# Optimization experiments

Hardware: AMD Instinct MI355X
Metric: run time of the kernel (lower is better)

## Reference

```python
import jax, jax.numpy as jnp
import numpy as np

B, S, H = 1, 2048, 4096
NH, DN, DR, DV = 32, 128, 64, 128   # heads, nope dim, rope dim, v dim
QK = DN + DR                         # 192
RQ, RKV = 1536, 512
EPS = 1e-6
NEG = jnp.float32(-1e9)


def rmsnorm(x, w, eps=EPS):
    x32 = x.astype(jnp.float32)
    var = jnp.mean(x32 * x32, axis=-1, keepdims=True)
    return (x32 * jax.lax.rsqrt(var + eps)).astype(x.dtype) * w


def rope_complex(x, cos, sin):
    # x: [..., S, D]; interpret adjacent pairs as complex, multiply by e^{i*theta}
    xr, xi = x[..., 0::2], x[..., 1::2]
    or_ = xr * cos - xi * sin
    oi_ = xr * sin + xi * cos
    return jnp.stack([or_, oi_], axis=-1).reshape(x.shape)


def setup_inputs() -> dict:
    key = jax.random.key(0)
    ks = jax.random.split(key, 8)
    std = 0.02
    # RoPE angles: theta_j = pos * base^{-2j/DR}, shape [B, S, DR/2]
    inv_freq = 1.0 / (10000.0 ** (np.arange(0, DR, 2, dtype=np.float32) / DR))
    pos = np.arange(S, dtype=np.float32)
    freqs = jnp.asarray(np.broadcast_to(pos[:, None] * inv_freq[None, :], (B, S, DR // 2)))
    return {
        "hidden_states": jax.random.normal(ks[0], (B, S, H), jnp.float32),
        "freqs": freqs,
        "q_a_w": jax.random.normal(ks[1], (RQ, H), jnp.float32) * std,
        "q_a_ln_w": jnp.ones((RQ,), jnp.float32),
        "q_b_w": jax.random.normal(ks[2], (NH * QK, RQ), jnp.float32) * std,
        "kv_a_w": jax.random.normal(ks[3], (RKV + DR, H), jnp.float32) * std,
        "kv_a_ln_w": jnp.ones((RKV,), jnp.float32),
        "kv_b_w": jax.random.normal(ks[4], (NH * (DN + DV), RKV), jnp.float32) * std,
        "o_w": jax.random.normal(ks[5], (H, NH * DV), jnp.float32) * std,
    }


def reference(hidden_states, freqs, q_a_w, q_a_ln_w, q_b_w, kv_a_w, kv_a_ln_w, kv_b_w, o_w):
    b, s, _ = hidden_states.shape
    # --- low-rank Q: hidden -> q_lora_rank -> heads*(nope+rope) ---
    q = rmsnorm(hidden_states @ q_a_w.T, q_a_ln_w) @ q_b_w.T          # [B,S,NH*QK]
    q = q.reshape(b, s, NH, QK).transpose(0, 2, 1, 3)                  # [B,NH,S,QK]
    q_pass, q_rot = q[..., :DN], q[..., DN:]                           # [B,NH,S,DN],[B,NH,S,DR]
    # --- compressed KV + shared rope key ---
    ckv = hidden_states @ kv_a_w.T                                     # [B,S,RKV+DR]
    k_pass_c, k_rot = ckv[..., :RKV], ckv[..., RKV:]
    kv = rmsnorm(k_pass_c, kv_a_ln_w) @ kv_b_w.T                       # [B,S,NH*(DN+DV)]
    kv = kv.reshape(b, s, NH, DN + DV).transpose(0, 2, 1, 3)           # [B,NH,S,DN+DV]
    k_pass, v = kv[..., :DN], kv[..., DN:]
    k_rot = k_rot.reshape(b, 1, s, DR)                                 # [B,1,S,DR]
    # --- decoupled RoPE (complex form) ---
    cos = jnp.cos(freqs)[:, None]                                      # [B,1,S,DR/2]
    sin = jnp.sin(freqs)[:, None]
    q_rot = rope_complex(q_rot, cos, sin)
    k_rot = rope_complex(k_rot, cos, sin)
    k_rot = jnp.broadcast_to(k_rot, (b, NH, s, DR))
    query = jnp.concatenate([q_pass, q_rot], axis=-1)                  # [B,NH,S,QK]
    key = jnp.concatenate([k_pass, k_rot], axis=-1)
    # --- causal attention ---
    scaling = QK ** -0.5
    scores = jnp.einsum("bhqd,bhkd->bhqk", query, key) * scaling
    causal = jnp.tril(jnp.ones((s, s), bool))
    scores = jnp.where(causal, scores, NEG)
    probs = jax.nn.softmax(scores.astype(jnp.float32), axis=-1).astype(query.dtype)
    out = jnp.einsum("bhqk,bhkd->bhqd", probs, v)                      # [B,NH,S,DV]
    out = out.transpose(0, 2, 1, 3).reshape(b, s, NH * DV)
    return out @ o_w.T                                                 # [B,S,H]
```

## Files before the change

### kernel.cpp

```cpp
#include <hip/hip_runtime.h>
#define S_LEN 2048
#define HDIM 4096
#define NHEAD 32
#define QKD 192
#define RQ_ 1536
#define CKV_W 576
#define KVW 8192
#define QFW 6144
#define SC2F 0.1041216313667742f

typedef float f32x4 __attribute__((ext_vector_type(4)));
typedef __bf16 bf16x8 __attribute__((ext_vector_type(8)));

__device__ __forceinline__ unsigned short f2bf(float f) {
  unsigned int u = __float_as_uint(f);
  u += 0x7fffu + ((u >> 16) & 1u);
  return (unsigned short)(u >> 16);
}
__device__ __forceinline__ float b2f(unsigned short u) {
  return __uint_as_float((unsigned int)u << 16);
}
__device__ __forceinline__ float ex2(float x) { return exp2f(x); }

__device__ __forceinline__ void stage16(const void* g, void* lds_base, int lane) {
  __builtin_amdgcn_global_load_lds(
      (const __attribute__((address_space(1))) unsigned int*)g,
      (__attribute__((address_space(3))) unsigned int*)lds_base, 16, 0, 0);
}

__global__ __launch_bounds__(256) void cvt_kernel(
    const float* __restrict__ in, unsigned short* __restrict__ out, int n8) {
  int i = blockIdx.x * 256 + threadIdx.x;
  if (i >= n8) return;
  const float4* p = reinterpret_cast<const float4*>(in) + (size_t)i * 2;
  float4 a = p[0], b = p[1];
  unsigned long long lo = (unsigned long long)f2bf(a.x) | ((unsigned long long)f2bf(a.y) << 16)
      | ((unsigned long long)f2bf(a.z) << 32) | ((unsigned long long)f2bf(a.w) << 48);
  unsigned long long hi = (unsigned long long)f2bf(b.x) | ((unsigned long long)f2bf(b.y) << 16)
      | ((unsigned long long)f2bf(b.z) << 32) | ((unsigned long long)f2bf(b.w) << 48);
  unsigned long long* q = reinterpret_cast<unsigned long long*>(out) + (size_t)i * 2;
  q[0] = lo; q[1] = hi;
}

template<bool BF16OUT, bool SPLITK, bool VSCAT>
__global__ __launch_bounds__(256) void gemm_bf(
    const unsigned short* __restrict__ A, int lda,
    const unsigned short* __restrict__ B, int ldb,
    void* __restrict__ Cv, int ldc, int N, int K,
    unsigned short* __restrict__ VtOut) {
  __shared__ unsigned short As[2][4][128][8];
  __shared__ unsigned short Bs[2][4][128][8];
  const int tid = threadIdx.x, lane = tid & 63, w = tid >> 6;
  const int gx = (int)gridDim.x, gy = (int)gridDim.y;
  const int nwg = gx * gy;
  int lin = (int)blockIdx.y * gx + (int)blockIdx.x;
  if ((nwg & 7) == 0) lin = (lin & 7) * (nwg >> 3) + (lin >> 3);
  const int bm = (lin % gy) * 128, bn = (lin / gy) * 128;
  const int koff = SPLITK ? (int)blockIdx.z * K : 0;
  const int wr = (w >> 1) * 64, wc = (w & 1) * 64;
  const int lg = lane >> 4, lm = lane & 15;
  f32x4 acc[4][4] = {};
  const int arow = bm + lane;
  int brow = bn + lane; if (brow >= N) brow = N - 1;

  auto STAGE = [&](int buf, int k0) {
#pragma unroll
    for (int i = 0; i < 2; ++i) {
      stage16(A + (size_t)(arow + i * 64) * lda + koff + k0 + w * 8, &As[buf][w][i * 64][0], lane);
      int br2 = brow + i * 64; if (br2 >= N) br2 = N - 1;
      stage16(B + (size_t)br2 * ldb + koff + k0 + w * 8, &Bs[buf][w][i * 64][0], lane);
    }
  };
  STAGE(0, 0);
  __syncthreads();
  int cur = 0;
  for (int k0 = 0; k0 < K; k0 += 32) {
    if (k0 + 32 < K) STAGE(cur ^ 1, k0 + 32);
    bf16x8 af[4], bf[4];
#pragma unroll
    for (int i = 0; i < 4; ++i)
      af[i] = *reinterpret_cast<const bf16x8*>(&As[cur][lg][wr + i * 16 + lm][0]);
#pragma unroll
    for (int j = 0; j < 4; ++j)
      bf[j] = *reinterpret_cast<const bf16x8*>(&Bs[cur][lg][wc + j * 16 + lm][0]);
    __builtin_amdgcn_s_setprio(1);
#pragma unroll
    for (int i = 0; i < 4; ++i)
#pragma unroll
      for (int j = 0; j < 4; ++j)
        acc[i][j] = __builtin_amdgcn_mfma_f32_16x16x32_bf16(af[i], bf[j], acc[i][j], 0, 0, 0);
    __builtin_amdgcn_s_setprio(0);
    __syncthreads();
    cur ^= 1;
  }

  if constexpr (VSCAT) {
    if (bn & 128) {
      const int h2 = bn >> 8;
#pragma unroll
      for (int i = 0; i < 4; ++i)
#pragma unroll
        for (int j = 0; j < 4; ++j) {
          int d = wc + j * 16 + lm;
          unsigned long long pk =
                (unsigned long long)f2bf(acc[i][j][0])
              | ((unsigned long long)f2bf(acc[i][j][1]) << 16)
              | ((unsigned long long)f2bf(acc[i][j][2]) << 32)
              | ((unsigned long long)f2bf(acc[i][j][3]) << 48);
          *reinterpret_cast<unsigned long long*>(
              VtOut + (size_t)(h2 * 128 + d) * S_LEN + bm + wr + i * 16 + lg * 4) = pk;
        }
      return;
    }
  }

  size_t zoff = SPLITK ? (size_t)blockIdx.z * S_LEN * N : 0;
#pragma unroll
  for (int i = 0; i < 4; ++i)
#pragma unroll
    for (int j = 0; j < 4; ++j)
#pragma unroll
      for (int r = 0; r < 4; ++r) {
        int row = bm + wr + i * 16 + lg * 4 + r;
        int col = bn + wc + j * 16 + lm;
        if (col < N) {
          if constexpr (BF16OUT)
            ((unsigned short*)Cv)[(size_t)row * ldc + col] = f2bf(acc[i][j][r]);
          else
            ((float*)Cv)[zoff + (size_t)row * ldc + col] = acc[i][j][r];
        }
      }
}

__global__ __launch_bounds__(256) void rms_sum_q(
    const float* __restrict__ P, const float* __restrict__ w,
    unsigned short* __restrict__ y) {
  __shared__ float red[4];
  const int row = blockIdx.x, tid = threadIdx.x;
  const float* base = P + (size_t)row * RQ_;
  float x[6]; float ss = 0.f;
#pragma unroll
  for (int ii = 0; ii < 6; ++ii) {
    int j = tid + ii * 256;
    float v = 0.f;
#pragma unroll
    for (int z = 0; z < 4; ++z) v += base[(size_t)z * S_LEN * RQ_ + j];
    x[ii] = v; ss += v * v;
  }
#pragma unroll
  for (int off = 1; off < 64; off <<= 1) ss += __shfl_xor(ss, off, 64);
  if ((tid & 63) == 0) red[tid >> 6] = ss;
  __syncthreads();
  float scale = rsqrtf((red[0] + red[1] + red[2] + red[3]) / (float)RQ_ + 1e-6f);
  unsigned short* q = y + (size_t)row * RQ_;
#pragma unroll
  for (int ii = 0; ii < 6; ++ii) {
    int j = tid + ii * 256;
    q[j] = f2bf(x[ii] * scale * w[j]);
  }
}

__global__ __launch_bounds__(256) void rms_sum_kv(
    const float* __restrict__ P, const float* __restrict__ w,
    unsigned short* __restrict__ y, float* __restrict__ rotf) {
  __shared__ float red[4];
  const int row = blockIdx.x, tid = threadIdx.x;
  const float* base = P + (size_t)row * CKV_W;
  float x0 = 0.f, x1 = 0.f, x2 = 0.f;
#pragma unroll
  for (int z = 0; z < 8; ++z) {
    const float* b = base + (size_t)z * S_LEN * CKV_W;
    x0 += b[tid]; x1 += b[tid + 256];
    if (tid < 64) x2 += b[tid + 512];
  }
  float ss = x0 * x0 + x1 * x1;
#pragma unroll
  for (int off = 1; off < 64; off <<= 1) ss += __shfl_xor(ss, off, 64);
  if ((tid & 63) == 0) red[tid >> 6] = ss;
  __syncthreads();
  float scale = rsqrtf((red[0] + red[1] + red[2] + red[3]) / 512.0f + 1e-6f);
  unsigned short* q = y + (size_t)row * 512;
  q[tid] = f2bf(x0 * scale * w[tid]);
  q[tid + 256] = f2bf(x1 * scale * w[tid + 256]);
  if (tid < 64) rotf[(size_t)row * 64 + tid] = x2;
}

__global__ __launch_bounds__(256) void rope_q_kernel(
    unsigned short* __restrict__ qf, const float* __restrict__ freqs) {
  int idx = blockIdx.x * 256 + threadIdx.x;
  if (idx >= NHEAD * S_LEN * 32) return;
  int r = idx & 31, s = (idx >> 5) & (S_LEN - 1), h = idx >> 16;
  unsigned short* p = qf + (size_t)s * QFW + h * QKD + 128 + 2 * r;
  float xr = b2f(p[0]), xi = b2f(p[1]);
  float f = freqs[(size_t)s * 32 + r];
  float c = cosf(f), sn = sinf(f);
  *reinterpret_cast<unsigned int*>(p) =
      (unsigned int)f2bf(xr * c - xi * sn) | ((unsigned int)f2bf(xr * sn + xi * c) << 16);
}

__global__ __launch_bounds__(256) void rope_k_kernel(
    const float* __restrict__ rotf, const float* __restrict__ freqs,
    unsigned short* __restrict__ Kr) {
  int idx = blockIdx.x * 256 + threadIdx.x;
  if (idx >= S_LEN * 32) return;
  int r = idx & 31, s = idx >> 5;
  float xr = rotf[(size_t)s * 64 + 2 * r];
  float xi = rotf[(size_t)s * 64 + 2 * r + 1];
  float f = freqs[(size_t)s * 32 + r];
  float c = cosf(f), sn = sinf(f);
  *reinterpret_cast<unsigned int*>(Kr + (size_t)s * 64 + 2 * r) =
      (unsigned int)f2bf(xr * c - xi * sn) | ((unsigned int)f2bf(xr * sn + xi * c) << 16);
}

__global__ __launch_bounds__(256, 3) void attn_kernel(
    const unsigned short* __restrict__ Qf,
    const unsigned short* __restrict__ KV,
    const unsigned short* __restrict__ Kr,
    const unsigned short* __restrict__ Vt,
    unsigned short* __restrict__ O) {
  __shared__ unsigned short Ks[2][32 * 192];
  __shared__ unsigned short Vs[2][128 * 32];
  __shared__ unsigned short Ps[4][16 * 32];
  const int tid = threadIdx.x, lane = tid & 63, w = tid >> 6;
  const int wg = (int)blockIdx.x;
  const int lin = (wg & 7) * 128 + (wg >> 3);
  const int h = lin >> 5;
  const int qt = 31 - (lin & 31);
  const int qr0 = qt * 64 + w * 16;
  const int lg = lane >> 4, lm = lane & 15, lm7 = lane & 7;
  const unsigned short* Qh = Qf + h * QKD;
  const int hoff = h * 256;
  const unsigned short* Vh = Vt + (size_t)h * 128 * S_LEN;

  bf16x8 qf[6];
#pragma unroll
  for (int f = 0; f < 6; ++f)
    qf[f] = *reinterpret_cast<const bf16x8*>(
        Qh + (size_t)(qr0 + lm) * QFW + f * 32 + lg * 8);

  f32x4 o[8] = {};
  float l[4] = {};

  auto STAGE = [&](int b, int kp) {
#pragma unroll
    for (int i = 0; i < 3; ++i) {
      int fb = (w * 3 + i) * 64 + lane;
      int row = fb / 24;
      int blk = fb - row * 24;
      int gb = (blk & ~7) | ((blk ^ row) & 7);
      const unsigned short* src = (blk < 16)
          ? KV + (size_t)(kp + row) * KVW + hoff + gb * 8
          : Kr + (size_t)(kp + row) * 64 + (gb - 16) * 8;
      stage16(src, &Ks[b][(w * 3 + i) * 512], lane);
    }
#pragma unroll
    for (int i = 0; i < 2; ++i) {
      int fb = (w * 2 + i) * 64 + lane;
      int row = fb >> 2;
      int blk = fb & 3;
      stage16(Vh + (size_t)row * S_LEN + kp + blk * 8, &Vs[b][(w * 2 + i) * 512], lane);
    }
  };

  const int ntiles = (qt + 1) * 2;
  STAGE(0, 0);
  __syncthreads();
  int buf = 0;
  for (int ti = 0; ti < ntiles; ++ti) {
    const int kp = ti * 32;
    if (ti + 1 < ntiles) STAGE(buf ^ 1, kp + 32);
    if (kp <= qr0 + 15) {
      f32x4 sc[2] = {};
      __builtin_amdgcn_s_setprio(1);
#pragma unroll
      for (int f = 0; f < 6; ++f)
#pragma unroll
        for (int c = 0; c < 2; ++c) {
          int blk = f * 4 + lg;
          int sb = (blk & ~7) | ((blk ^ lm7) & 7);
          bf16x8 kf = *reinterpret_cast<const bf16x8*>(&Ks[buf][(c * 16 + lm) * 192 + sb * 8]);
          sc[c] = __builtin_amdgcn_mfma_f32_16x16x32_bf16(qf[f], kf, sc[c], 0, 0, 0);
        }
      __builtin_amdgcn_s_setprio(0);
      const int rb = qr0 + lg * 4;
#pragma unroll
      for (int r = 0; r < 4; ++r) {
        const int row = rb + r;
        float v0 = fmaf(sc[0][r], SC2F, -32.f); if (kp + lm > row) v0 = -1e9f;
        float v1 = fmaf(sc[1][r], SC2F, -32.f); if (kp + 16 + lm > row) v1 = -1e9f;
        float p0 = ex2(v0), p1 = ex2(v1);
        l[r] += p0 + p1;
        int pr = lg * 4 + r;
        int s3 = pr & 3;
        int b0 = lm >> 3;
        unsigned short* pp = &Ps[w][pr * 32];
        pp[((b0 ^ s3) << 3) + lm7] = f2bf(p0);
        pp[(((2 + b0) ^ s3) << 3) + lm7] = f2bf(p1);
      }
      bf16x8 pa = *reinterpret_cast<const bf16x8*>(
          &Ps[w][lm * 32 + ((lg ^ (lm & 3)) << 3)]);
      __builtin_amdgcn_s_setprio(1);
#pragma unroll
      for (int d = 0; d < 8; ++d) {
        bf16x8 vf = *reinterpret_cast<const bf16x8*>(&Vs[buf][(d * 16 + lm) * 32 + lg * 8]);
        o[d] = __builtin_amdgcn_mfma_f32_16x16x32_bf16(pa, vf, o[d], 0, 0, 0);
      }
      __builtin_amdgcn_s_setprio(0);
    }
    __syncthreads();
    buf ^= 1;
  }
#pragma unroll
  for (int r = 0; r < 4; ++r) {
    float t = l[r];
#pragma unroll
    for (int off = 1; off < 16; off <<= 1) t += __shfl_xor(t, off, 16);
    float inv = 1.0f / t;
    int row = qr0 + lg * 4 + r;
#pragma unroll
    for (int d = 0; d < 8; ++d)
      O[(size_t)row * 4096 + h * 128 + d * 16 + lm] = f2bf(o[d][r] * inv);
  }
}

extern "C" void kernel_launch(void* const* d_in, const int* in_sizes, int n_in,
                              void* d_out, int out_size, void* d_ws, size_t ws_size,
                              hipStream_t stream) {
  const float* hs = (const float*)d_in[0];
  const float* freqs = (const float*)d_in[1];
  const float* q_a_w = (const float*)d_in[2];
  const float* q_a_ln = (const float*)d_in[3];
  const float* q_b_w = (const float*)d_in[4];
  const float* kv_a_w = (const float*)d_in[5];
  const float* kv_a_ln = (const float*)d_in[6];
  const float* kv_b_w = (const float*)d_in[7];
  const float* o_w = (const float*)d_in[8];
  float* out = (float*)d_out;

  char* ws = (char*)d_ws;
  unsigned short* wslot = (unsigned short*)(ws + 0);
  unsigned short* hs_bf = (unsigned short*)(ws + 33554432);
  unsigned short* attnb = (unsigned short*)(ws + 33554432);
  float* qa_part = (float*)(ws + 50331648);
  unsigned short* kv_bf = (unsigned short*)(ws + 50331648);
  float* ckv_part = (float*)(ws + 100663296);
  unsigned short* qa_bf = (unsigned short*)(ws + 138412032);
  unsigned short* ckv_bf = (unsigned short*)(ws + 144703488);
  float* rotf = (float*)(ws + 146800640);
  unsigned short* qfullb = (unsigned short*)(ws + 147324928);
  unsigned short* Vt = (unsigned short*)(ws + 172490752);
  unsigned short* Kr = (unsigned short*)(ws + 189267968);

  dim3 blk(256);
  auto cvt = [&](const float* src, unsigned short* dst, size_t n) {
    int n8 = (int)(n / 8);
    cvt_kernel<<<(n8 + 255) / 256, blk, 0, stream>>>(src, dst, n8);
  };

  cvt(hs, hs_bf, (size_t)S_LEN * HDIM);
  cvt(q_a_w, wslot, (size_t)RQ_ * HDIM);
  gemm_bf<false, true, false><<<dim3(RQ_ / 128, S_LEN / 128, 4), blk, 0, stream>>>(
      hs_bf, HDIM, wslot, HDIM, qa_part, RQ_, RQ_, HDIM / 4, nullptr);
  cvt(kv_a_w, wslot, (size_t)CKV_W * HDIM);
  gemm_bf<false, true, false><<<dim3((CKV_W + 127) / 128, S_LEN / 128, 8), blk, 0, stream>>>(
      hs_bf, HDIM, wslot, HDIM, ckv_part, CKV_W, CKV_W, HDIM / 8, nullptr);
  rms_sum_q<<<S_LEN, blk, 0, stream>>>(qa_part, q_a_ln, qa_bf);
  rms_sum_kv<<<S_LEN, blk, 0, stream>>>(ckv_part, kv_a_ln, ckv_bf, rotf);
  cvt(q_b_w, wslot, (size_t)QFW * RQ_);
  gemm_bf<true, false, false><<<dim3(QFW / 128, S_LEN / 128), blk, 0, stream>>>(
      qa_bf, RQ_, wslot, RQ_, qfullb, QFW, QFW, RQ_, nullptr);
  cvt(kv_b_w, wslot, (size_t)KVW * 512);
  gemm_bf<true, false, true><<<dim3(KVW / 128, S_LEN / 128), blk, 0, stream>>>(
      ckv_bf, 512, wslot, 512, kv_bf, KVW, KVW, 512, Vt);
  rope_q_kernel<<<(NHEAD * S_LEN * 32 + 255) / 256, blk, 0, stream>>>(qfullb, freqs);
  rope_k_kernel<<<(S_LEN * 32 + 255) / 256, blk, 0, stream>>>(rotf, freqs, Kr);
  attn_kernel<<<dim3(1024), blk, 0, stream>>>(qfullb, kv_bf, Kr, Vt, attnb);
  cvt(o_w, wslot, (size_t)HDIM * HDIM);
  gemm_bf<false, false, false><<<dim3(HDIM / 128, S_LEN / 128), blk, 0, stream>>>(
      attnb, HDIM, wslot, HDIM, out, HDIM, HDIM, HDIM, nullptr);
}
```

Measured before the change: 523.7 us.

## Merge q_a and kv_a projections into one split-K GEMM and fuse k-rope into rmsnorm

Concatenates the q_a and kv_a weights in the workspace so a single split-K GEMM (17 column tiles, 4 K-splits) computes both low-rank projections into one partial buffer. The KV normalisation kernel now applies RoPE to the shared rope key directly using a lane shuffle, which removes the separate rope_k kernel and its fp32 intermediate. This cuts kernel launches and fills the GPU better than two small GEMMs. In exchange, the kv part now uses 4 K-splits instead of 8, and the last column tile is partially masked.

```diff
diff --git a/kernel.cpp b/kernel.cpp
--- a/kernel.cpp
+++ b/kernel.cpp
@@ -5,6 +5,7 @@
 #define QKD 192
 #define RQ_ 1536
 #define CKV_W 576
+#define NQKV 2112
 #define KVW 8192
 #define QFW 6144
 #define SC2F 0.1041216313667742f
@@ -137,14 +138,14 @@
     unsigned short* __restrict__ y) {
   __shared__ float red[4];
   const int row = blockIdx.x, tid = threadIdx.x;
-  const float* base = P + (size_t)row * RQ_;
+  const float* base = P + (size_t)row * NQKV;
   float x[6]; float ss = 0.f;
 #pragma unroll
   for (int ii = 0; ii < 6; ++ii) {
     int j = tid + ii * 256;
     float v = 0.f;
 #pragma unroll
-    for (int z = 0; z < 4; ++z) v += base[(size_t)z * S_LEN * RQ_ + j];
+    for (int z = 0; z < 4; ++z) v += base[(size_t)z * S_LEN * NQKV + j];
     x[ii] = v; ss += v * v;
   }
 #pragma unroll
@@ -162,14 +163,15 @@
 
 __global__ __launch_bounds__(256) void rms_sum_kv(
     const float* __restrict__ P, const float* __restrict__ w,
-    unsigned short* __restrict__ y, float* __restrict__ rotf) {
+    const float* __restrict__ freqs,
+    unsigned short* __restrict__ y, unsigned short* __restrict__ Kr) {
   __shared__ float red[4];
   const int row = blockIdx.x, tid = threadIdx.x;
-  const float* base = P + (size_t)row * CKV_W;
+  const float* base = P + (size_t)row * NQKV + RQ_;
   float x0 = 0.f, x1 = 0.f, x2 = 0.f;
 #pragma unroll
-  for (int z = 0; z < 8; ++z) {
-    const float* b = base + (size_t)z * S_LEN * CKV_W;
+  for (int z = 0; z < 4; ++z) {
+    const float* b = base + (size_t)z * S_LEN * NQKV;
     x0 += b[tid]; x1 += b[tid + 256];
     if (tid < 64) x2 += b[tid + 512];
   }
@@ -182,7 +184,15 @@
   unsigned short* q = y + (size_t)row * 512;
   q[tid] = f2bf(x0 * scale * w[tid]);
   q[tid + 256] = f2bf(x1 * scale * w[tid + 256]);
-  if (tid < 64) rotf[(size_t)row * 64 + tid] = x2;
+  if (tid < 64) {
+    float part = __shfl_xor(x2, 1, 64);
+    int r = tid >> 1;
+    float f = freqs[(size_t)row * 32 + r];
+    float c = cosf(f), sn = sinf(f);
+    float out = (tid & 1) ? (part * sn + x2 * c)
+                          : (x2 * c - part * sn);
+    Kr[(size_t)row * 64 + tid] = f2bf(out);
+  }
 }
 
 __global__ __launch_bounds__(256) void rope_q_kernel(
@@ -195,20 +205,6 @@
   float f = freqs[(size_t)s * 32 + r];
   float c = cosf(f), sn = sinf(f);
   *reinterpret_cast<unsigned int*>(p) =
-      (unsigned int)f2bf(xr * c - xi * sn) | ((unsigned int)f2bf(xr * sn + xi * c) << 16);
-}
-
-__global__ __launch_bounds__(256) void rope_k_kernel(
-    const float* __restrict__ rotf, const float* __restrict__ freqs,
-    unsigned short* __restrict__ Kr) {
-  int idx = blockIdx.x * 256 + threadIdx.x;
-  if (idx >= S_LEN * 32) return;
-  int r = idx & 31, s = idx >> 5;
-  float xr = rotf[(size_t)s * 64 + 2 * r];
-  float xi = rotf[(size_t)s * 64 + 2 * r + 1];
-  float f = freqs[(size_t)s * 32 + r];
-  float c = cosf(f), sn = sinf(f);
-  *reinterpret_cast<unsigned int*>(Kr + (size_t)s * 64 + 2 * r) =
       (unsigned int)f2bf(xr * c - xi * sn) | ((unsigned int)f2bf(xr * sn + xi * c) << 16);
 }
 
@@ -341,12 +337,10 @@
   unsigned short* wslot = (unsigned short*)(ws + 0);
   unsigned short* hs_bf = (unsigned short*)(ws + 33554432);
   unsigned short* attnb = (unsigned short*)(ws + 33554432);
-  float* qa_part = (float*)(ws + 50331648);
+  float* qkv_part = (float*)(ws + 50331648);
   unsigned short* kv_bf = (unsigned short*)(ws + 50331648);
-  float* ckv_part = (float*)(ws + 100663296);
   unsigned short* qa_bf = (unsigned short*)(ws + 138412032);
   unsigned short* ckv_bf = (unsigned short*)(ws + 144703488);
-  float* rotf = (float*)(ws + 146800640);
   unsigned short* qfullb = (unsigned short*)(ws + 147324928);
   unsigned short* Vt = (unsigned short*)(ws + 172490752);
   unsigned short* Kr = (unsigned short*)(ws + 189267968);
@@ -359,13 +353,11 @@
 
   cvt(hs, hs_bf, (size_t)S_LEN * HDIM);
   cvt(q_a_w, wslot, (size_t)RQ_ * HDIM);
-  gemm_bf<false, true, false><<<dim3(RQ_ / 128, S_LEN / 128, 4), blk, 0, stream>>>(
-      hs_bf, HDIM, wslot, HDIM, qa_part, RQ_, RQ_, HDIM / 4, nullptr);
-  cvt(kv_a_w, wslot, (size_t)CKV_W * HDIM);
-  gemm_bf<false, true, false><<<dim3((CKV_W + 127) / 128, S_LEN / 128, 8), blk, 0, stream>>>(
-      hs_bf, HDIM, wslot, HDIM, ckv_part, CKV_W, CKV_W, HDIM / 8, nullptr);
-  rms_sum_q<<<S_LEN, blk, 0, stream>>>(qa_part, q_a_ln, qa_bf);
-  rms_sum_kv<<<S_LEN, blk, 0, stream>>>(ckv_part, kv_a_ln, ckv_bf, rotf);
+  cvt(kv_a_w, wslot + (size_t)RQ_ * HDIM, (size_t)CKV_W * HDIM);
+  gemm_bf<false, true, false><<<dim3(17, S_LEN / 128, 4), blk, 0, stream>>>(
+      hs_bf, HDIM, wslot, HDIM, qkv_part, NQKV, NQKV, HDIM / 4, nullptr);
+  rms_sum_q<<<S_LEN, blk, 0, stream>>>(qkv_part, q_a_ln, qa_bf);
+  rms_sum_kv<<<S_LEN, blk, 0, stream>>>(qkv_part, kv_a_ln, freqs, ckv_bf, Kr);
   cvt(q_b_w, wslot, (size_t)QFW * RQ_);
   gemm_bf<true, false, false><<<dim3(QFW / 128, S_LEN / 128), blk, 0, stream>>>(
       qa_bf, RQ_, wslot, RQ_, qfullb, QFW, QFW, RQ_, nullptr);
@@ -373,7 +365,6 @@
   gemm_bf<true, false, true><<<dim3(KVW / 128, S_LEN / 128), blk, 0, stream>>>(
       ckv_bf, 512, wslot, 512, kv_bf, KVW, KVW, 512, Vt);
   rope_q_kernel<<<(NHEAD * S_LEN * 32 + 255) / 256, blk, 0, stream>>>(qfullb, freqs);
-  rope_k_kernel<<<(S_LEN * 32 + 255) / 256, blk, 0, stream>>>(rotf, freqs, Kr);
   attn_kernel<<<dim3(1024), blk, 0, stream>>>(qfullb, kv_bf, Kr, Vt, attnb);
   cvt(o_w, wslot, (size_t)HDIM * HDIM);
   gemm_bf<false, false, false><<<dim3(HDIM / 128, S_LEN / 128), blk, 0, stream>>>(
```

After: 519.2 us. About the same (-0.9%).
